# Optimization experiments

Measured on AMD Instinct MI355X. Metric: run time of the kernel, lower is better.

## Reference

```python
import jax, jax.numpy as jnp
import numpy as np

# Static config matching init_kwargs: T_horizon=5.0, dt=0.1 -> N_T = int(5.0/0.1)
N_T = 50
SAT_SCALE = 5.0  # saturate_cbf: h = (sigmoid(h/5)-0.5)*2*5


def braking_controller(state):
    # state: [B, A, 4] = (x, y, v, theta)
    brake = -((jax.nn.sigmoid(state[..., 2] * 4.0) - 0.5) * 2.0 * 9.0)[..., None]
    turn = jnp.zeros_like(brake)
    return jnp.concatenate([brake, turn], axis=-1)  # [B, A, 2]


def unicycle_step(state, u, dt):
    # Euler step of unicycle dynamics; state=(x,y,v,theta), u=(accel,yawrate), dt:[B,A,1]
    v, th = state[..., 2], state[..., 3]
    dxdt = jnp.concatenate(
        [(v * jnp.cos(th))[..., None], (v * jnp.sin(th))[..., None], u], axis=-1)
    return state + dt * dxdt


def rotate2d(p, ang):
    # rotate 2D points p[...,2] by angle ang[...]
    c, s = jnp.cos(ang), jnp.sin(ang)
    return jnp.stack([c * p[..., 0] - s * p[..., 1],
                      s * p[..., 0] + c * p[..., 1]], axis=-1)


def veh_veh_distance(ego, agents, ego_extent, agent_extent):
    # ego, agents: [B,A,T,3]; extents: [B,A,1,3] (L,W,H). Rectangle-vs-disc
    # separation evaluated in both body frames (tbsim-style VEH_VEH_distance).
    rel1 = rotate2d(agents[..., :2] - ego[..., :2], -ego[..., 2])
    rel2 = rotate2d(ego[..., :2] - agents[..., :2], -agents[..., 2])
    r_ag = 0.5 * jnp.linalg.norm(agent_extent[..., :2], axis=-1, keepdims=True)
    r_eg = 0.5 * jnp.linalg.norm(ego_extent[..., :2], axis=-1, keepdims=True)
    dis1 = jnp.abs(rel1) - 0.5 * ego_extent[..., :2] - r_ag
    dis2 = jnp.abs(rel2) - 0.5 * agent_extent[..., :2] - r_eg
    return jnp.maximum(dis1.max(-1), dis2.max(-1))  # [B, A, T]


def reference(data):
    # data: [B, A, 15]
    ego0 = data[..., 0:4]
    ag0 = data[..., 4:8]
    ego_ext = data[..., 8:11]
    ag_ext = data[..., 11:14]
    dt = data[..., 14:15]  # [B, A, 1]

    def step(carry, _):
        ego, ag = carry
        ego = unicycle_step(ego, braking_controller(ego), dt)
        ag = unicycle_step(ag, braking_controller(ag), dt)
        return (ego, ag), (ego, ag)

    _, (ego_traj, ag_traj) = jax.lax.scan(step, (ego0, ag0), None, length=N_T)
    ego_traj = jnp.moveaxis(ego_traj, 0, 2)  # [B, A, T, 4]
    ag_traj = jnp.moveaxis(ag_traj, 0, 2)

    dist = veh_veh_distance(ego_traj[..., 0:3], ag_traj[..., 0:3],
                            ego_ext[..., None, :], ag_ext[..., None, :])  # [B,A,T]
    h = dist.min(-1)  # min over the forward horizon -> [B, A]
    # saturate_cbf
    return (jax.nn.sigmoid(h / SAT_SCALE) - 0.5) * 2.0 * SAT_SCALE


def setup_inputs() -> dict:
    B, A = 1024, 64
    key = jax.random.key(0)
    k1, k2, k3 = jax.random.split(key, 3)
    states = jax.random.normal(k1, (B, A, 8), dtype=jnp.float32)
    # spread out positions, keep v/theta O(1)
    scale = jnp.array([10., 10., 3., 1., 10., 10., 3., 1.], dtype=jnp.float32)
    states = states * scale
    # positive, realistic extents (L~4, W~2, H~1.5) for ego and agent
    base_ext = jnp.array([4., 2., 1.5, 4., 2., 1.5], dtype=jnp.float32)
    ext = base_ext + 0.3 * jnp.abs(jax.random.normal(k2, (B, A, 6), dtype=jnp.float32))
    dt = jnp.full((B, A, 1), 0.1, dtype=jnp.float32)
    data = jnp.concatenate([states, ext, dt], axis=-1)  # [B, A, 15]
    return {"data": data}
```

## Files before the change

### kernel.cpp

```cpp
#include <hip/hip_runtime.h>

#define N_T 50

__device__ __forceinline__ float tanh_fast(float x) {
    x = fminf(20.0f, fmaxf(-20.0f, x));
    float e = __expf(-2.0f * x);
    return (1.0f - e) / (1.0f + e);
}

__global__ __launch_bounds__(256)
void cbf_kernel(const float* __restrict__ data, float* __restrict__ out, int n) {
    __shared__ float lds[256 * 15];
    const int tid  = threadIdx.x;
    const int base = blockIdx.x * 256;
    const int cnt  = min(256, n - base);
    {
        const float* src = data + (long long)base * 15;
        const int total = cnt * 15;
        for (int k = tid; k < total; k += 256) lds[k] = src[k];
    }
    __syncthreads();
    if (tid >= cnt) return;
    const float* d = &lds[tid * 15];

    float ex = d[0],  ey = d[1],  ev = d[2],  eth = d[3];
    float ax = d[4],  ay = d[5],  av = d[6],  ath = d[7];
    float eex = d[8], eey = d[9];
    float aex = d[11], aey = d[12];
    float dt = d[14];

    const float r_ag = 0.5f * sqrtf(aex * aex + aey * aey);
    const float r_eg = 0.5f * sqrtf(eex * eex + eey * eey);
    const float hex = 0.5f * eex, hey = 0.5f * eey;
    const float hax = 0.5f * aex, hay = 0.5f * aey;

    float ce, se; __sincosf(eth, &se, &ce);
    float ca, sa; __sincosf(ath, &sa, &ca);

    float hmin = 3.4e38f;
    #pragma unroll 2
    for (int t = 0; t < N_T; ++t) {
        float bke = -9.0f * tanh_fast(2.0f * ev);
        float bka = -9.0f * tanh_fast(2.0f * av);
        ex = fmaf(dt * ev, ce, ex);
        ey = fmaf(dt * ev, se, ey);
        ax = fmaf(dt * av, ca, ax);
        ay = fmaf(dt * av, sa, ay);
        ev = fmaf(dt, bke, ev);
        av = fmaf(dt, bka, av);

        float dx = ax - ex, dy = ay - ey;
        float c1, s1; __sincosf(ev, &s1, &c1);
        float c2, s2; __sincosf(av, &s2, &c2);
        float rx1 = fmaf(c1, dx,  s1 * dy);
        float ry1 = fmaf(c1, dy, -s1 * dx);
        float rx2 = fmaf(-c2, dx, -s2 * dy);
        float ry2 = fmaf(c2, -dy,  s2 * dx);

        float d1 = fmaxf(fabsf(rx1) - hex, fabsf(ry1) - hey) - r_ag;
        float d2 = fmaxf(fabsf(rx2) - hax, fabsf(ry2) - hay) - r_eg;
        hmin = fminf(hmin, fmaxf(d1, d2));
    }

    out[base + tid] = 5.0f * tanh_fast(0.1f * hmin);
}

extern "C" void kernel_launch(void* const* d_in, const int* in_sizes, int n_in,
                              void* d_out, int out_size, void* d_ws, size_t ws_size,
                              hipStream_t stream) {
    const float* data = (const float*)d_in[0];
    float* out = (float*)d_out;
    const int n = in_sizes[0] / 15;
    const int blocks = (n + 255) / 256;
    cbf_kernel<<<blocks, 256, 0, stream>>>(data, out, n);
}
```

Measured before the change: 62.68 us.

## Split ego and agent rollouts across paired lanes with shuffle exchange

Each element is now handled by two adjacent threads: one integrates the ego and the other the agent. Positions and the per-frame distance are swapped between the pair with lane shuffles. This halves the serial dependency chain per thread and doubles the thread count (512 blocks of 256 threads), which should raise latency hiding. It also replaces the divide in tanh with a hardware reciprocal and folds dt into constants. The cost is three cross-lane shuffles per timestep, and half the lanes sit idle during the final store.

```diff
diff --git a/kernel.cpp b/kernel.cpp
--- a/kernel.cpp
+++ b/kernel.cpp
@@ -2,67 +2,69 @@
 
 #define N_T 50
 
-__device__ __forceinline__ float tanh_fast(float x) {
-    x = fminf(20.0f, fmaxf(-20.0f, x));
-    float e = __expf(-2.0f * x);
-    return (1.0f - e) / (1.0f + e);
+__device__ __forceinline__ float tanh2_fast(float v) {
+    float e = __expf(fminf(-4.0f * v, 80.0f));
+    return (1.0f - e) * __builtin_amdgcn_rcpf(1.0f + e);
 }
 
 __global__ __launch_bounds__(256)
 void cbf_kernel(const float* __restrict__ data, float* __restrict__ out, int n) {
-    __shared__ float lds[256 * 15];
-    const int tid  = threadIdx.x;
-    const int base = blockIdx.x * 256;
-    const int cnt  = min(256, n - base);
+    const int EPB = 128;
+    __shared__ float lds[EPB * 15];
+    const int tid   = threadIdx.x;
+    const int ebase = blockIdx.x * EPB;
+    const int cnt   = min(EPB, n - ebase);
     {
-        const float* src = data + (long long)base * 15;
+        const float* src = data + (long long)ebase * 15;
         const int total = cnt * 15;
         for (int k = tid; k < total; k += 256) lds[k] = src[k];
     }
     __syncthreads();
-    if (tid >= cnt) return;
-    const float* d = &lds[tid * 15];
 
-    float ex = d[0],  ey = d[1],  ev = d[2],  eth = d[3];
-    float ax = d[4],  ay = d[5],  av = d[6],  ath = d[7];
-    float eex = d[8], eey = d[9];
-    float aex = d[11], aey = d[12];
+    const int e   = tid >> 1;
+    const int odd = tid & 1;
+    if (e >= cnt) return;
+    const float* d  = &lds[e * 15];
+    const float* st = d + odd * 4;
+    const float* xt = d + 8 + odd * 3;
+
+    float x  = st[0], y = st[1], v = st[2], th = st[3];
+    float ex = xt[0], ey = xt[1];
     float dt = d[14];
 
-    const float r_ag = 0.5f * sqrtf(aex * aex + aey * aey);
-    const float r_eg = 0.5f * sqrtf(eex * eex + eey * eey);
-    const float hex = 0.5f * eex, hey = 0.5f * eey;
-    const float hax = 0.5f * aex, hay = 0.5f * aey;
+    const float hx = 0.5f * ex, hy = 0.5f * ey;
+    const float r_self    = 0.5f * sqrtf(ex * ex + ey * ey);
+    const float r_partner = __shfl_xor(r_self, 1);
 
-    float ce, se; __sincosf(eth, &se, &ce);
-    float ca, sa; __sincosf(ath, &sa, &ca);
+    const float kc   = dt * __cosf(th);
+    const float ks   = dt * __sinf(th);
+    const float n9dt = -9.0f * dt;
 
     float hmin = 3.4e38f;
     #pragma unroll 2
     for (int t = 0; t < N_T; ++t) {
-        float bke = -9.0f * tanh_fast(2.0f * ev);
-        float bka = -9.0f * tanh_fast(2.0f * av);
-        ex = fmaf(dt * ev, ce, ex);
-        ey = fmaf(dt * ev, se, ey);
-        ax = fmaf(dt * av, ca, ax);
-        ay = fmaf(dt * av, sa, ay);
-        ev = fmaf(dt, bke, ev);
-        av = fmaf(dt, bka, av);
+        float tb = tanh2_fast(v);
+        x = fmaf(v, kc, x);
+        y = fmaf(v, ks, y);
+        v = fmaf(n9dt, tb, v);
 
-        float dx = ax - ex, dy = ay - ey;
-        float c1, s1; __sincosf(ev, &s1, &c1);
-        float c2, s2; __sincosf(av, &s2, &c2);
-        float rx1 = fmaf(c1, dx,  s1 * dy);
-        float ry1 = fmaf(c1, dy, -s1 * dx);
-        float rx2 = fmaf(-c2, dx, -s2 * dy);
-        float ry2 = fmaf(c2, -dy,  s2 * dx);
+        float px = __shfl_xor(x, 1);
+        float py = __shfl_xor(y, 1);
+        float dx = px - x, dy = py - y;
 
-        float d1 = fmaxf(fabsf(rx1) - hex, fabsf(ry1) - hey) - r_ag;
-        float d2 = fmaxf(fabsf(rx2) - hax, fabsf(ry2) - hay) - r_eg;
-        hmin = fminf(hmin, fmaxf(d1, d2));
+        float sv = __sinf(v), cv = __cosf(v);
+        float rx = fmaf(cv, dx,  sv * dy);
+        float ry = fmaf(cv, dy, -sv * dx);
+
+        float ds_ = fmaxf(fabsf(rx) - hx, fabsf(ry) - hy) - r_partner;
+        float dp  = fmaxf(ds_, __shfl_xor(ds_, 1));
+        hmin = fminf(hmin, dp);
     }
 
-    out[base + tid] = 5.0f * tanh_fast(0.1f * hmin);
+    if (!odd) {
+        float e2 = __expf(fminf(-0.2f * hmin, 80.0f));
+        out[ebase + e] = 5.0f * (1.0f - e2) * __builtin_amdgcn_rcpf(1.0f + e2);
+    }
 }
 
 extern "C" void kernel_launch(void* const* d_in, const int* in_sizes, int n_in,
@@ -71,6 +73,7 @@
     const float* data = (const float*)d_in[0];
     float* out = (float*)d_out;
     const int n = in_sizes[0] / 15;
-    const int blocks = (n + 255) / 256;
+    const int EPB = 128;
+    const int blocks = (n + EPB - 1) / EPB;
     cbf_kernel<<<blocks, 256, 0, stream>>>(data, out, n);
 }
```

New measurement: 60.27 us. -3.8%, faster.
